# Kernel optimization log

Hardware: AMD Instinct MI355X
Metric: run time of the kernel (lower is better)

The kernel has to match this reference:

```python
import jax, jax.numpy as jnp
import numpy as np

SCALE = 1000.0
NEG = -1000000000.0
B, S, T, E, H = 64, 512, 96, 256, 512  # batch, src_len, trg_len, embed_dim, hidden_dim
ENC_DIM = 2 * H


def setup_inputs() -> dict:
    key = jax.random.key(0)
    def rn(i, shape):
        return jax.random.normal(jax.random.fold_in(key, i), shape, jnp.float32) / np.sqrt(shape[-1])
    inp = {}
    inp["src"] = jax.random.uniform(jax.random.fold_in(key, 100), (B, S), jnp.float32, 50.0, 1500.0)
    src_len = jax.random.randint(jax.random.fold_in(key, 101), (B,), S // 2, S + 1)
    inp["src_mask"] = (jnp.arange(S)[None, :] < src_len[:, None]).astype(jnp.int32)
    trg = jax.random.uniform(jax.random.fold_in(key, 102), (B, T), jnp.float32, 50.0, 1500.0)
    inp["trg"] = trg.at[:, 0].set(0.0)  # position 0 is the start sentinel
    trg_len = jax.random.randint(jax.random.fold_in(key, 103), (B,), T // 2, T + 1)
    inp["trg_mask"] = (jnp.arange(T)[None, :] < trg_len[:, None]).astype(jnp.int32)
    shapes = {
        "enc_proj_W": (E, 1), "enc_proj_b": (E,),
        "enc_Wih_f": (4 * H, E), "enc_Whh_f": (4 * H, H), "enc_bih_f": (4 * H,), "enc_bhh_f": (4 * H,),
        "enc_Wih_b": (4 * H, E), "enc_Whh_b": (4 * H, H), "enc_bih_b": (4 * H,), "enc_bhh_b": (4 * H,),
        "fc_h_W": (H, 2 * H), "fc_h_b": (H,), "fc_c_W": (H, 2 * H), "fc_c_b": (H,),
        "dec_proj_W": (E, 1), "dec_proj_b": (E,),
        "attn_Wenc": (H, ENC_DIM), "attn_Wdec": (H, H), "attn_v": (1, H),
        "dec_Wih": (4 * H, E + ENC_DIM), "dec_Whh": (4 * H, H), "dec_bih": (4 * H,), "dec_bhh": (4 * H,),
        "val_W": (1, H + ENC_DIM + E), "val_b": (1,),
        "stop_W": (1, H + ENC_DIM + E), "stop_b": (1,),
    }
    for i, (name, shp) in enumerate(shapes.items()):
        inp[name] = rn(i, shp)
    return inp


def _lstm_scan(x_tbe, m_tb1, Wih, Whh, bih, bhh, reverse):
    # Mask-gated LSTM scan == pack_padded_sequence semantics (padding at end):
    # state is frozen and outputs zeroed at padded steps; reverse=True gives the
    # backward direction of the bidirectional encoder.
    b, h = x_tbe.shape[1], Whh.shape[1]
    init = (jnp.zeros((b, h), x_tbe.dtype), jnp.zeros((b, h), x_tbe.dtype))
    bias = bih + bhh
    def step(carry, xm):
        hprev, cprev = carry
        xt, m = xm
        gates = xt @ Wih.T + hprev @ Whh.T + bias  # [B,4H], torch gate order i,f,g,o
        i, f, g, o = jnp.split(gates, 4, axis=-1)
        c_new = jax.nn.sigmoid(f) * cprev + jax.nn.sigmoid(i) * jnp.tanh(g)
        h_new = jax.nn.sigmoid(o) * jnp.tanh(c_new)
        hn = jnp.where(m, h_new, hprev)
        cn = jnp.where(m, c_new, cprev)
        return (hn, cn), jnp.where(m, h_new, 0.0)
    (hT, cT), outs = jax.lax.scan(step, init, (x_tbe, m_tb1), reverse=reverse)
    return outs, hT, cT


def _forward(src, trg, enc_proj_W, enc_proj_b, enc_Wih_f, enc_Whh_f, enc_bih_f, enc_bhh_f, enc_Wih_b, enc_Whh_b, enc_bih_b, enc_bhh_b, fc_h_W, fc_h_b, fc_c_W, fc_c_b, dec_proj_W, dec_proj_b, attn_Wenc, attn_Wdec, attn_v, dec_Wih, dec_Whh, dec_bih, dec_bhh, val_W, val_b, stop_W, stop_b, src_mask, trg_mask):
    src_norm = src / SCALE
    # ---- encoder (bidirectional, n_layers=1, dropout inactive in eval) ----
    emb = src_norm[..., None] * enc_proj_W[:, 0] + enc_proj_b  # Linear(1,E) -> [B,S,E]
    emb_t = jnp.transpose(emb, (1, 0, 2))                      # [S,B,E] time-major
    m_t = (src_mask.T > 0)[..., None]                          # [S,B,1]
    out_f, hF, cF = _lstm_scan(emb_t, m_t, enc_Wih_f, enc_Whh_f, enc_bih_f, enc_bhh_f, False)
    out_b, hB, cB = _lstm_scan(emb_t, m_t, enc_Wih_b, enc_Whh_b, enc_bih_b, enc_bhh_b, True)
    enc_outputs = jnp.transpose(jnp.concatenate([out_f, out_b], -1), (1, 0, 2))  # [B,S,2H]
    hidden = jnp.tanh(jnp.concatenate([hF, hB], -1) @ fc_h_W.T + fc_h_b)  # [B,H]
    cell = jnp.tanh(jnp.concatenate([cF, cB], -1) @ fc_c_W.T + fc_c_b)    # [B,H]
    # ---- decoder loop (full teacher forcing, ratio=1.0) ----
    eh = enc_outputs @ attn_Wenc.T  # [B,S,H], loop-invariant (same math, hoisted)
    valid = src_mask > 0            # [B,S]
    dec_bias = dec_bih + dec_bhh
    def dec_step(carry, x_t):
        h, c = carry
        energy = jnp.tanh((h @ attn_Wdec.T)[:, None, :] + eh)  # [B,S,H]
        scores = jnp.where(valid, energy @ attn_v[0], NEG)     # [B,S]
        w = jax.nn.softmax(scores, axis=1)
        context = jnp.einsum('bs,bse->be', w, enc_outputs)     # [B,2H]
        e = x_t[:, None] * dec_proj_W[:, 0] + dec_proj_b       # [B,E]
        gates = jnp.concatenate([e, context], -1) @ dec_Wih.T + h @ dec_Whh.T + dec_bias
        i, f, g, o = jnp.split(gates, 4, axis=-1)
        c_new = jax.nn.sigmoid(f) * c + jax.nn.sigmoid(i) * jnp.tanh(g)
        h_new = jax.nn.sigmoid(o) * jnp.tanh(c_new)
        feat = jnp.concatenate([h_new, context, e], -1)        # [B, H+2H+E]
        pv = feat @ val_W[0] + val_b[0]
        sl = feat @ stop_W[0] + stop_b[0]
        return (h_new, c_new), (pv * SCALE, sl)
    dec_in = (trg[:, :-1] / SCALE).T  # [T-1,B]: inputs for steps t=1..trg_len-1
    _, (pred_values, stop_logits) = jax.lax.scan(dec_step, (hidden, cell), dec_in)
    return pred_values.T, stop_logits.T  # each [B, T-1]


def reference(src, src_mask, trg, trg_mask, enc_proj_W, enc_proj_b, enc_Wih_f, enc_Whh_f, enc_bih_f, enc_bhh_f, enc_Wih_b, enc_Whh_b, enc_bih_b, enc_bhh_b, fc_h_W, fc_h_b, fc_c_W, fc_c_b, dec_proj_W, dec_proj_b, attn_Wenc, attn_Wdec, attn_v, dec_Wih, dec_Whh, dec_bih, dec_bhh, val_W, val_b, stop_W, stop_b):
    return _forward(src, trg, enc_proj_W, enc_proj_b, enc_Wih_f, enc_Whh_f, enc_bih_f, enc_bhh_f, enc_Wih_b, enc_Whh_b, enc_bih_b, enc_bhh_b, fc_h_W, fc_h_b, fc_c_W, fc_c_b, dec_proj_W, dec_proj_b, attn_Wenc, attn_Wdec, attn_v, dec_Wih, dec_Whh, dec_bih, dec_bhh, val_W, val_b, stop_W, stop_b, src_mask, trg_mask)
```

## Files before the change

kernel.cpp:

```cpp
#include <hip/hip_runtime.h>
#include <hip/hip_bf16.h>

#define AGENT __HIP_MEMORY_SCOPE_AGENT

typedef float f32x4 __attribute__((ext_vector_type(4)));
typedef short short8 __attribute__((ext_vector_type(8)));
union V16 { f32x4 f; short8 s; };


__device__ __forceinline__ float sigm(float x){ return 1.f/(1.f+__expf(-x)); }
__device__ __forceinline__ float tanhfast(float x){
  float ax = fabsf(x);
  float e = __expf(-2.f*ax);
  float r = (1.f-e)/(1.f+e);
  return copysignf(r, x);
}
__device__ __forceinline__ float dot4(float4 a, float4 b){
  return fmaf(a.x,b.x, fmaf(a.y,b.y, fmaf(a.z,b.z, a.w*b.w)));
}
__device__ __forceinline__ unsigned short bfbits(float x){
  return __bfloat16_as_ushort(__float2bfloat16(x));
}
__device__ __forceinline__ float bfu2f(unsigned short u){
  union{unsigned v; float f;} x; x.v = ((unsigned)u)<<16; return x.f;
}

__global__ void __launch_bounds__(256) precompute(
  const float* __restrict__ Wenc,
  const float* __restrict__ Wihf, const float* __restrict__ epW, const float* __restrict__ epb,
  const float* __restrict__ bihf, const float* __restrict__ bhhf,
  const float* __restrict__ Wihb, const float* __restrict__ bihb, const float* __restrict__ bhhb,
  const float* __restrict__ dWih, const float* __restrict__ dpW, const float* __restrict__ dpb,
  const float* __restrict__ dbih, const float* __restrict__ dbhh,
  const float* __restrict__ valW, const float* __restrict__ valb,
  const float* __restrict__ stopW, const float* __restrict__ stopb,
  float* __restrict__ PQ, float* __restrict__ WT, float* __restrict__ hc)
{
  const int idx = blockIdx.x*256 + threadIdx.x;
  if (idx < 524288){
    const int j = idx >> 9, n = idx & 511;
    WT[idx] = Wenc[(size_t)n*1024 + j];
  } else if (idx < 524288 + 6*2048){
    const int q = idx - 524288;
    const int set = q >> 11, j = q & 2047;
    const float* row; const float* vec; float add = 0.f;
    switch(set){
      case 0: row = Wihf + (size_t)j*256; vec = epW; break;
      case 1: row = Wihf + (size_t)j*256; vec = epb; add = bihf[j]+bhhf[j]; break;
      case 2: row = Wihb + (size_t)j*256; vec = epW; break;
      case 3: row = Wihb + (size_t)j*256; vec = epb; add = bihb[j]+bhhb[j]; break;
      case 4: row = dWih + (size_t)j*1280; vec = dpW; break;
      default: row = dWih + (size_t)j*1280; vec = dpb; add = dbih[j]+dbhh[j]; break;
    }
    float a = add;
    for (int e=0;e<256;e++) a = fmaf(row[e], vec[e], a);
    PQ[set*2048 + j] = a;
  } else if (idx < 524288 + 6*2048 + 4){
    const int q = idx - (524288 + 6*2048);
    const float* wrow = (q<2) ? valW : stopW;
    const float* vec  = (q&1) ? dpb : dpW;
    float a = (q&1) ? ((q<2)? valb[0] : stopb[0]) : 0.f;
    for (int e=0;e<256;e++) a = fmaf(wrow[1536+e], vec[e], a);
    hc[q] = a;
  }
}

__global__ void __launch_bounds__(512) wconv(
  const float* __restrict__ Whhf, const float* __restrict__ Whhb,
  const float* __restrict__ dWih, const float* __restrict__ dWhh,
  const float* __restrict__ Wdec, const float* __restrict__ Wenc,
  unsigned short* __restrict__ Wbf, unsigned short* __restrict__ Wcat,
  unsigned short* __restrict__ Wdecb, unsigned short* __restrict__ Wencb)
{
  const int i = blockIdx.x*512 + threadIdx.x;
  if (i < 2097152){
    const float v = (i < 1048576) ? Whhf[i] : Whhb[i-1048576];
    Wbf[i] = bfbits(v);
  } else if (i < 2097152+3145728){
    const int q = i - 2097152;
    const int r = q/1536, k = q - r*1536;
    const float v = (k<1024) ? dWih[(size_t)r*1280 + 256 + k] : dWhh[(size_t)r*512 + (k-1024)];
    Wcat[q] = bfbits(v);
  } else if (i < 2097152+3145728+262144){
    const int q = i - (2097152+3145728);
    Wdecb[q] = bfbits(Wdec[q]);
  } else if (i < 2097152+3145728+262144+524288){
    const int q = i - (2097152+3145728+262144);
    Wencb[q] = bfbits(Wenc[q]);
  }
}

__global__ void __launch_bounds__(512) enc_mfma(
    const float* __restrict__ src, const int* __restrict__ smask,
    const unsigned short* __restrict__ Wbf,
    const float* __restrict__ PQ,
    unsigned short* __restrict__ hbuf,
    float* __restrict__ hfin,
    float* __restrict__ cf, float* __restrict__ cb,
    __hip_bfloat16* __restrict__ enc,
    unsigned* __restrict__ cnt)
{
  __shared__ float hlds[16*256];
  __shared__ float red[4*64*4];
  __shared__ float gbuf[4*256];
  __shared__ alignas(16) unsigned short hstage[256];
  __shared__ alignas(16) unsigned short estage[256];

  const int tid = threadIdx.x;
  const int bid = blockIdx.x;
  const int dir = bid>>7, bhalf = (bid>>5)&3, us = bid&31;
  const int b0 = bhalf*16;
  unsigned* gcnt = cnt + (dir*4 + bhalf)*32;
  const int wv = tid>>6, lane = tid&63;
  const int nt = wv&3, kh = wv>>2;
  const int rowb = lane&15;

  short8 bfr[8];
  {
    const int g = nt*512 + us*16 + (lane&15);
    const unsigned short* wp = Wbf + ((size_t)dir*2048 + g)*512 + kh*256 + (lane>>4)*8;
    #pragma unroll
    for (int kt=0;kt<8;kt++) bfr[kt] = *(const short8*)(wp + kt*32);
  }

  float p0=0,p1=0,p2=0,p3=0,q0=0,q1=0,q2=0,q3=0;
  float creg = 0.f, hprev = 0.f;
  int bg = 0, ug = 0;
  if (tid < 256){
    bg = b0 + (tid>>4);
    ug = us*16 + (tid&15);
    const float* P = PQ + dir*4096; const float* Q = P + 2048;
    p0=P[ug]; p1=P[ug+512]; p2=P[ug+1024]; p3=P[ug+1536];
    q0=Q[ug]; q1=Q[ug+512]; q2=Q[ug+1024]; q3=Q[ug+1536];
  }

  for (int tt=0; tt<512; ++tt){
    const int t = dir ? (511-tt) : tt;
    if (tt>0){
      if (tid==0){
        while (__hip_atomic_load(gcnt, __ATOMIC_RELAXED, AGENT) < 32u*(unsigned)tt)
          __builtin_amdgcn_s_sleep(1);
      }
      __syncthreads();
      const int par = (tt-1)&1;
      f32x4 tmp0, tmp1;
      {
        const int f0 = tid, f1 = 512 + tid;
        const unsigned short* g0 = hbuf + (((size_t)(dir*2+par)*64 + b0 + (f0>>6))<<9) + (f0&63)*8;
        const unsigned short* g1 = hbuf + (((size_t)(dir*2+par)*64 + b0 + (f1>>6))<<9) + (f1&63)*8;
        asm volatile("global_load_dwordx4 %0, %1, off sc0 sc1" : "=v"(tmp0) : "v"(g0) : "memory");
        asm volatile("global_load_dwordx4 %0, %1, off sc0 sc1" : "=v"(tmp1) : "v"(g1) : "memory");
      }
      asm volatile("s_waitcnt vmcnt(0)" ::: "memory");
      __builtin_amdgcn_sched_barrier(0);
      {
        const int r0 = tid>>6, c0 = tid&63;
        *(f32x4*)&hlds[r0*256 + ((c0 ^ (r0&7))<<2)] = tmp0;
        const int r1 = (512+tid)>>6, c1 = tid&63;
        *(f32x4*)&hlds[r1*256 + ((c1 ^ (r1&7))<<2)] = tmp1;
      }
      __syncthreads();
    }

    f32x4 acc = {0.f,0.f,0.f,0.f};
    if (tt>0){
      #pragma unroll
      for (int kt=0; kt<8; ++kt){
        const int ch = (kh*8 + kt)*4 + (lane>>4);
        V16 a; a.f = *(const f32x4*)&hlds[rowb*256 + ((ch ^ (rowb&7))<<2)];
        acc = __builtin_amdgcn_mfma_f32_16x16x32_bf16(a.s, bfr[kt], acc, 0, 0, 0);
      }
    }
    if (kh==1) *(f32x4*)&red[(nt*64+lane)*4] = acc;
    __syncthreads();
    if (kh==0){
      const f32x4 o = *(const f32x4*)&red[(nt*64+lane)*4];
      #pragma unroll
      for (int i=0;i<4;i++){
        const int r = (lane>>4)*4 + i, c = lane&15;
        gbuf[nt*256 + r*16 + c] = acc[i] + o[i];
      }
    }
    __syncthreads();

    if (tid < 256){
      const float sx = src[bg*512+t]*0.001f;
      const int m = smask[bg*512+t];
      const float gi = gbuf[0*256+tid] + sx*p0 + q0;
      const float gf = gbuf[1*256+tid] + sx*p1 + q1;
      const float gg = gbuf[2*256+tid] + sx*p2 + q2;
      const float go = gbuf[3*256+tid] + sx*p3 + q3;
      const float cn = fmaf(sigm(gf), creg, sigm(gi)*tanhfast(gg));
      const float hn = sigm(go)*tanhfast(cn);
      const float hk = m ? hn : hprev;
      creg = m ? cn : creg;
      hprev = hk;
      hstage[tid] = bfbits(hk);
      estage[tid] = bfbits(m ? hn : 0.f);
    }
    __syncthreads();
    if (tid < 32){
      const int row = tid>>1, hw = tid&1;
      const f32x4 v = *(const f32x4*)(hstage + row*16 + hw*8);
      unsigned short* dst = hbuf + (((size_t)(dir*2+(tt&1))*64 + b0 + row)<<9) + us*16 + hw*8;
      asm volatile("global_store_dwordx4 %0, %1, off sc0 sc1" :: "v"(dst), "v"(v) : "memory");
    } else if (tid < 64){
      const int j = tid-32, row = j>>1, hw = j&1;
      const f32x4 v = *(const f32x4*)(estage + row*16 + hw*8);
      *(f32x4*)((unsigned short*)enc + ((size_t)((b0+row)*512 + t))*1024 + dir*512 + us*16 + hw*8) = v;
    }
    asm volatile("s_waitcnt vmcnt(0)" ::: "memory");
    __syncthreads();
    if (tid==0) __hip_atomic_fetch_add(gcnt, 1u, __ATOMIC_RELAXED, AGENT);
  }

  if (tid < 256){
    hfin[dir*32768 + bg*512 + ug] = hprev;
    (dir ? cb : cf)[bg*512 + ug] = creg;
  }
}

__global__ void __launch_bounds__(256) fc_init(
  const float* __restrict__ hf0, const float* __restrict__ hb0,
  const float* __restrict__ cf, const float* __restrict__ cb,
  const float* __restrict__ fchW, const float* __restrict__ fchB,
  const float* __restrict__ fccW, const float* __restrict__ fccB,
  float* __restrict__ dech, float* __restrict__ decc)
{
  const int which = blockIdx.x >> 7;
  const int wid = blockIdx.x & 127;
  const int b = threadIdx.x >> 2, ul = threadIdx.x & 3;
  const int u = wid*4 + ul;
  const float* s0 = which ? cf : hf0;
  const float* s1 = which ? cb : hb0;
  const float* W = which ? fccW : fchW;
  float acc = (which ? fccB : fchB)[u];
  const float4* x0 = (const float4*)(s0 + b*512);
  const float4* x1 = (const float4*)(s1 + b*512);
  const float4* wr = (const float4*)(W + (size_t)u*1024);
  #pragma unroll 4
  for (int k=0;k<128;k++) acc += dot4(x0[k], wr[k]);
  #pragma unroll 4
  for (int k=0;k<128;k++) acc += dot4(x1[k], wr[128+k]);
  (which ? decc : dech)[b*512+u] = tanhfast(acc);
}

__global__ void __launch_bounds__(256) eh_mfma(
  const unsigned short* __restrict__ enc,
  const unsigned short* __restrict__ Wencb,
  unsigned short* __restrict__ eh2)
{
  const int b = blockIdx.x>>6, st = (blockIdx.x>>3)&7, nt0 = blockIdx.x&7;
  const int wv = threadIdx.x>>6, lane = threadIdx.x&63;
  const int sA = st*64 + wv*16 + (lane&15);
  const int kb = (lane>>4)*8;
  const unsigned short* ap  = enc + ((size_t)(b*512 + sA))*1024 + kb;
  const unsigned short* bp0 = Wencb + ((size_t)(nt0*64 + (lane&15)))*1024 + kb;
  f32x4 acc[4] = {{0,0,0,0},{0,0,0,0},{0,0,0,0},{0,0,0,0}};
  for (int k0=0; k0<1024; k0+=32){
    V16 a; a.f = *(const f32x4*)(ap + k0);
    #pragma unroll
    for (int nt=0; nt<4; ++nt){
      V16 bb; bb.f = *(const f32x4*)(bp0 + (size_t)nt*16*1024 + k0);
      acc[nt] = __builtin_amdgcn_mfma_f32_16x16x32_bf16(a.s, bb.s, acc[nt], 0, 0, 0);
    }
  }
  const int sO = st*64 + wv*16 + (lane>>4)*4;
  const int col = lane&15;
  #pragma unroll
  for (int nt=0; nt<4; ++nt){
    #pragma unroll
    for (int i=0;i<4;i++){
      eh2[((size_t)(b*512 + sO + i))*512 + nt0*64 + nt*16 + col] = bfbits(acc[nt][i]);
    }
  }
}

__global__ void __launch_bounds__(256) enc_tr(
  const unsigned short* __restrict__ enc, unsigned short* __restrict__ encT2)
{
  __shared__ unsigned short tl[64][80];
  const int b = blockIdx.x>>7, st = (blockIdx.x>>4)&7, jt = blockIdx.x&15;
  const int r = threadIdx.x>>2, q = threadIdx.x&3;
  const unsigned short* src = enc + ((size_t)(b*512 + st*64 + r))*1024 + jt*64 + q*16;
  *(short8*)&tl[r][q*16]   = *(const short8*)src;
  *(short8*)&tl[r][q*16+8] = *(const short8*)(src+8);
  __syncthreads();
  unsigned short tmp[16];
  #pragma unroll
  for (int e=0;e<16;e++) tmp[e] = tl[q*16+e][r];
  unsigned short* dst = encT2 + ((size_t)(b*1024 + jt*64 + r))*512 + st*64 + q*16;
  *(short8*)dst     = *(short8*)&tmp[0];
  *(short8*)(dst+8) = *(short8*)&tmp[8];
}

template<int NG>
__device__ __forceinline__ void gbar(unsigned* gctr, unsigned* root, int grp, unsigned gen){
  asm volatile("s_waitcnt vmcnt(0)" ::: "memory");
  __syncthreads();
  if (threadIdx.x==0){
    const unsigned old = __hip_atomic_fetch_add(gctr + grp*32, 1u, __ATOMIC_RELAXED, AGENT);
    if (old == gen*16u - 1u)
      __hip_atomic_fetch_add(root, 1u, __ATOMIC_RELAXED, AGENT);
    while (__hip_atomic_load(root, __ATOMIC_RELAXED, AGENT) < gen*(unsigned)NG)
      __builtin_amdgcn_s_sleep(1);
  }
  __syncthreads();
}
template<int NB>
__device__ __forceinline__ void mbar(unsigned* mc, unsigned mgen){
  asm volatile("s_waitcnt vmcnt(0)" ::: "memory");
  __syncthreads();
  if (threadIdx.x==0){
    __hip_atomic_fetch_add(mc, 1u, __ATOMIC_RELAXED, AGENT);
    while (__hip_atomic_load(mc, __ATOMIC_RELAXED, AGENT) < mgen*(unsigned)NB)
      __builtin_amdgcn_s_sleep(1);
  }
  __syncthreads();
}

__global__ void __launch_bounds__(512) dec_fused256(
  const float* __restrict__ trg, const int* __restrict__ smask,
  const float* __restrict__ attnv,
  const unsigned short* __restrict__ eh2,
  const unsigned short* __restrict__ encT2,
  const unsigned short* __restrict__ Wcat,
  const unsigned short* __restrict__ Wdecb,
  const float* __restrict__ PQd, const float* __restrict__ hc,
  const float* __restrict__ valW, const float* __restrict__ stopW,
  const float* __restrict__ dech0, const float* __restrict__ decc0,
  float* __restrict__ scorep, float* __restrict__ ctxf,
  unsigned short* __restrict__ xbuf, float* __restrict__ gates,
  float* __restrict__ hcur, float* __restrict__ out,
  unsigned* __restrict__ gctr, unsigned* __restrict__ root, unsigned* __restrict__ mctr)
{
  __shared__ alignas(16) float redl[8192];
  __shared__ float vlds[512];
  __shared__ float hldsa[512];
  __shared__ float adhl[128];
  __shared__ float wlds[512];
  const int tid = threadIdx.x;
  const int bid = blockIdx.x;
  const int b = bid>>2, quad = bid&3;
  const int grp = bid>>4;
  const int lane = tid&63, wv = tid>>6;
  unsigned* mc = mctr + b*32;
  unsigned g = 0, m = 0;

  vlds[tid] = attnv[tid];

  short8 gw[6];
  if (bid < 128){
    const int n = bid*16 + (lane&15);
    const unsigned short* wp = Wcat + (size_t)n*1536 + wv*192 + (lane>>4)*8;
    #pragma unroll
    for (int ks=0;ks<6;ks++) gw[ks] = *(const short8*)(wp + ks*32);
  }

  const bool isb = (quad==0);
  float hr=0.f, cr=0.f;
  float pqi=0,pqf=0,pqg=0,pqo=0, qqi=0,qqf=0,qqg=0,qqo=0;
  float vwh=0,vwc0=0,vwc1=0, swh=0,swc0=0,swc1=0;
  if (isb){
    hr = dech0[b*512+tid]; cr = decc0[b*512+tid];
    pqi = PQd[tid];      pqf = PQd[512+tid];      pqg = PQd[1024+tid];      pqo = PQd[1536+tid];
    qqi = PQd[2048+tid]; qqf = PQd[2048+512+tid]; qqg = PQd[2048+1024+tid]; qqo = PQd[2048+1536+tid];
    vwh = valW[tid]; vwc0 = valW[512+tid]; vwc1 = valW[1024+tid];
    swh = stopW[tid]; swc0 = stopW[512+tid]; swc1 = stopW[1024+tid];
  }

  if (isb){
    const unsigned hb16 = (unsigned)bfbits(hr);
    unsigned short* xp = xbuf + b*1536 + 1024 + tid;
    asm volatile("global_store_short %0, %1, off sc0 sc1" :: "v"(xp), "v"(hb16) : "memory");
    float* hp = hcur + b*512 + tid;
    asm volatile("global_store_dword %0, %1, off sc0 sc1" :: "v"(hp), "v"(hr) : "memory");
  }
  ++m; mbar<4>(mc, m);

  for (int t=0; t<95; ++t){
    {
      float hv; const float* hp = hcur + b*512 + tid;
      asm volatile("global_load_dword %0, %1, off sc0 sc1\ns_waitcnt vmcnt(0)" : "=v"(hv) : "v"(hp) : "memory");
      hldsa[tid] = hv;
      __syncthreads();
      {
        const int jl = tid>>2, uc = tid&3;
        const unsigned short* wp = Wdecb + (size_t)(quad*128 + jl)*512 + uc*128;
        float a = 0.f;
        #pragma unroll
        for (int i=0;i<16;i++){
          const short8 w8 = *(const short8*)(wp + i*8);
          #pragma unroll
          for (int e=0;e<8;e++)
            a = fmaf(hldsa[uc*128 + i*8 + e], bfu2f((unsigned short)w8[e]), a);
        }
        redl[tid] = a;
      }
      __syncthreads();
      if (tid < 128)
        adhl[tid] = redl[tid*4] + redl[tid*4+1] + redl[tid*4+2] + redl[tid*4+3];
      __syncthreads();
      {
        const unsigned short* ep = eh2 + ((size_t)(b*512 + tid))*512 + quad*128;
        float part = 0.f;
        #pragma unroll
        for (int i=0;i<16;i++){
          const short8 e8 = *(const short8*)(ep + i*8);
          #pragma unroll
          for (int e=0;e<8;e++){
            const int n = i*8 + e;
            part = fmaf(vlds[quad*128+n], tanhfast(adhl[n] + bfu2f((unsigned short)e8[e])), part);
          }
        }
        float* sp = scorep + (size_t)bid*512 + tid;
        asm volatile("global_store_dword %0, %1, off sc0 sc1" :: "v"(sp), "v"(part) : "memory");
      }
    }
    ++m; mbar<4>(mc, m);

    {
      float pa, pb, pc, pd;
      const float* pp = scorep + (size_t)(b*4)*512 + tid;
      asm volatile("global_load_dword %0, %1, off sc0 sc1" : "=v"(pa) : "v"(pp) : "memory");
      asm volatile("global_load_dword %0, %1, off sc0 sc1" : "=v"(pb) : "v"(pp+512) : "memory");
      asm volatile("global_load_dword %0, %1, off sc0 sc1" : "=v"(pc) : "v"(pp+1024) : "memory");
      asm volatile("global_load_dword %0, %1, off sc0 sc1" : "=v"(pd) : "v"(pp+1536) : "memory");
      asm volatile("s_waitcnt vmcnt(0)" ::: "memory");
      __builtin_amdgcn_sched_barrier(0);
      float s0 = (pa+pb)+(pc+pd);
      s0 = smask[b*512+tid] ? s0 : -1.0e9f;
      redl[512+tid] = s0;
      __syncthreads();
      for (int off=256; off>0; off>>=1){
        if (tid<off) redl[512+tid] = fmaxf(redl[512+tid], redl[512+tid+off]);
        __syncthreads();
      }
      const float mx = redl[512];
      __syncthreads();
      const float e = __expf(s0 - mx);
      redl[512+tid] = e;
      __syncthreads();
      for (int off=256; off>0; off>>=1){
        if (tid<off) redl[512+tid] += redl[512+tid+off];
        __syncthreads();
      }
      const float Z = redl[512];
      __syncthreads();
      wlds[tid] = e / Z;
      __syncthreads();
      {
        const int jj = tid>>1, sh = tid&1;
        const unsigned short* cp = encT2 + ((size_t)(b*1024 + quad*256 + jj))*512 + sh*256;
        float c = 0.f;
        #pragma unroll
        for (int i=0;i<32;i++){
          const short8 c8 = *(const short8*)(cp + i*8);
          #pragma unroll
          for (int e2=0;e2<8;e2++)
            c = fmaf(wlds[sh*256 + i*8 + e2], bfu2f((unsigned short)c8[e2]), c);
        }
        redl[tid] = c;
      }
      __syncthreads();
      if (tid < 256){
        const float cv = redl[tid*2] + redl[tid*2+1];
        const int j = quad*256 + tid;
        float* cp2 = ctxf + b*1024 + j;
        asm volatile("global_store_dword %0, %1, off sc0 sc1" :: "v"(cp2), "v"(cv) : "memory");
        const unsigned cb16 = (unsigned)bfbits(cv);
        unsigned short* xp = xbuf + b*1536 + j;
        asm volatile("global_store_short %0, %1, off sc0 sc1" :: "v"(xp), "v"(cb16) : "memory");
      }
    }
    ++g; gbar<16>(gctr, root, grp, g);

    if (bid < 128){
      f32x4 av[2][6];
      f32x4 acc[4] = {{0,0,0,0},{0,0,0,0},{0,0,0,0},{0,0,0,0}};
      {
        const unsigned short* xp0 = xbuf + (size_t)(lane&15)*1536 + wv*192 + (lane>>4)*8;
        #pragma unroll
        for (int ks=0;ks<6;ks++){
          const unsigned short* p = xp0 + ks*32;
          asm volatile("global_load_dwordx4 %0, %1, off sc0 sc1" : "=v"(av[0][ks]) : "v"(p) : "memory");
        }
      }
      #pragma unroll
      for (int mt=0; mt<4; ++mt){
        if (mt<3){
          const unsigned short* xpn = xbuf + (size_t)((mt+1)*16 + (lane&15))*1536 + wv*192 + (lane>>4)*8;
          #pragma unroll
          for (int ks=0;ks<6;ks++){
            const unsigned short* p = xpn + ks*32;
            asm volatile("global_load_dwordx4 %0, %1, off sc0 sc1" : "=v"(av[(mt+1)&1][ks]) : "v"(p) : "memory");
          }
          asm volatile("s_waitcnt vmcnt(6)" ::: "memory");
        } else {
          asm volatile("s_waitcnt vmcnt(0)" ::: "memory");
        }
        __builtin_amdgcn_sched_barrier(0);
        #pragma unroll
        for (int ks=0;ks<6;ks++){
          V16 a; a.f = av[mt&1][ks];
          acc[mt] = __builtin_amdgcn_mfma_f32_16x16x32_bf16(a.s, gw[ks], acc[mt], 0, 0, 0);
        }
      }
      #pragma unroll
      for (int mt=0; mt<4; ++mt)
        *(f32x4*)&redl[wv*1024 + lane*16 + mt*4] = acc[mt];
    }
    __syncthreads();
    if (bid < 128){
      #pragma unroll
      for (int h2=0; h2<2; ++h2){
        const int o = h2*512 + tid;
        const int ob = o>>4, col = o&15;
        const int mt = ob>>4, row = ob&15;
        const int base = (((row>>2)<<4) | col)*16 + mt*4 + (row&3);
        float gsum = 0.f;
        #pragma unroll
        for (int w2=0; w2<8; ++w2) gsum += redl[w2*1024 + base];
        float* gp = gates + ob*2048 + bid*16 + col;
        asm volatile("global_store_dword %0, %1, off sc0 sc1" :: "v"(gp), "v"(gsum) : "memory");
      }
    }
    ++g; gbar<16>(gctr, root, grp, g);

    if (isb){
      float g4[4], c0v, c1v;
      {
        const float* gp = gates + b*2048 + tid;
        const float* cp = ctxf + b*1024 + tid;
        asm volatile("global_load_dword %0, %1, off sc0 sc1" : "=v"(g4[0]) : "v"(gp) : "memory");
        asm volatile("global_load_dword %0, %1, off sc0 sc1" : "=v"(g4[1]) : "v"(gp+512) : "memory");
        asm volatile("global_load_dword %0, %1, off sc0 sc1" : "=v"(g4[2]) : "v"(gp+1024) : "memory");
        asm volatile("global_load_dword %0, %1, off sc0 sc1" : "=v"(g4[3]) : "v"(gp+1536) : "memory");
        asm volatile("global_load_dword %0, %1, off sc0 sc1" : "=v"(c0v) : "v"(cp) : "memory");
        asm volatile("global_load_dword %0, %1, off sc0 sc1" : "=v"(c1v) : "v"(cp+512) : "memory");
        asm volatile("s_waitcnt vmcnt(0)" ::: "memory");
        __builtin_amdgcn_sched_barrier(0);
      }
      const float x = trg[b*96 + t]*0.001f;
      const float gi = g4[0] + x*pqi + qqi;
      const float gf = g4[1] + x*pqf + qqf;
      const float gg = g4[2] + x*pqg + qqg;
      const float go = g4[3] + x*pqo + qqo;
      const float cn = fmaf(sigm(gf), cr, sigm(gi)*tanhfast(gg));
      const float hn = sigm(go)*tanhfast(cn);
      cr = cn; hr = hn;
      const unsigned hb16 = (unsigned)bfbits(hn);
      unsigned short* xp = xbuf + b*1536 + 1024 + tid;
      asm volatile("global_store_short %0, %1, off sc0 sc1" :: "v"(xp), "v"(hb16) : "memory");
      float* hp = hcur + b*512 + tid;
      asm volatile("global_store_dword %0, %1, off sc0 sc1" :: "v"(hp), "v"(hn) : "memory");
      redl[512+tid]  = fmaf(hn, vwh, fmaf(c0v, vwc0, c1v*vwc1));
      redl[1024+tid] = fmaf(hn, swh, fmaf(c0v, swc0, c1v*swc1));
      __syncthreads();
      for (int off=256; off>0; off>>=1){
        if (tid<off){ redl[512+tid]+=redl[512+tid+off]; redl[1024+tid]+=redl[1024+tid+off]; }
        __syncthreads();
      }
      if (tid==0){
        out[b*95 + t] = (redl[512] + x*hc[0] + hc[1])*1000.f;
        out[6080 + b*95 + t] = redl[1024] + x*hc[2] + hc[3];
      }
    }
    ++m; mbar<4>(mc, m);
  }
}

__global__ void __launch_bounds__(512, 4) dec_fused512(
  const float* __restrict__ trg, const int* __restrict__ smask,
  const float* __restrict__ attnv,
  const unsigned short* __restrict__ eh2,
  const unsigned short* __restrict__ encT2,
  const unsigned short* __restrict__ Wcat,
  const unsigned short* __restrict__ Wdecb,
  const float* __restrict__ PQd, const float* __restrict__ hc,
  const float* __restrict__ valW, const float* __restrict__ stopW,
  const float* __restrict__ dech0, const float* __restrict__ decc0,
  float* __restrict__ scorep, float* __restrict__ ctxf,
  unsigned short* __restrict__ xbuf, float* __restrict__ gates,
  float* __restrict__ hcur, float* __restrict__ out,
  unsigned* __restrict__ gctr, unsigned* __restrict__ root, unsigned* __restrict__ mctr)
{
  __shared__ unsigned short eh2l[32768];
  __shared__ alignas(16) float redl[2048];
  __shared__ float vlds[512];
  __shared__ float adhl[64];
  __shared__ int slen_sh;
  const int tid = threadIdx.x;
  const int bid = blockIdx.x;
  const int b = bid>>3, oct = bid&7;
  const int grp = bid>>4;
  const int lane = tid&63, wv = tid>>6;
  unsigned* mc = mctr + b*32;
  unsigned g = 0, m = 0;

  vlds[tid] = attnv[tid];

  redl[tid] = (float)smask[b*512+tid];
  __syncthreads();
  for (int off=256; off>0; off>>=1){
    if (tid<off) redl[tid] += redl[tid+off];
    __syncthreads();
  }
  if (tid==0) slen_sh = (int)(redl[0]+0.5f);
  __syncthreads();
  const int slen = slen_sh;
  const int nch = (slen + 127) >> 7;

  {
    const unsigned short* ep = eh2 + ((size_t)(b*512 + tid))*512 + oct*64;
    short8 r8[8];
    #pragma unroll
    for (int i=0;i<8;i++) r8[i] = *(const short8*)(ep + i*8);
    #pragma unroll
    for (int i=0;i<8;i++)
      #pragma unroll
      for (int e=0;e<8;e++)
        eh2l[(i*8+e)*512 + tid] = (unsigned short)r8[i][e];
  }
  __syncthreads();

  short8 gw[6];
  if (bid < 128){
    const int n = bid*16 + (lane&15);
    const unsigned short* wp = Wcat + (size_t)n*1536 + wv*192 + (lane>>4)*8;
    #pragma unroll
    for (int ks=0;ks<6;ks++) gw[ks] = *(const short8*)(wp + ks*32);
  }

  const bool isb = (oct==0);
  float hr=0.f, cr=0.f;
  float pqi=0,pqf=0,pqg=0,pqo=0, qqi=0,qqf=0,qqg=0,qqo=0;
  float vwh=0,vwc0=0,vwc1=0, swh=0,swc0=0,swc1=0;
  if (isb){
    hr = dech0[b*512+tid]; cr = decc0[b*512+tid];
    pqi = PQd[tid];      pqf = PQd[512+tid];      pqg = PQd[1024+tid];      pqo = PQd[1536+tid];
    qqi = PQd[2048+tid]; qqf = PQd[2048+512+tid]; qqg = PQd[2048+1024+tid]; qqo = PQd[2048+1536+tid];
    vwh = valW[tid]; vwc0 = valW[512+tid]; vwc1 = valW[1024+tid];
    swh = stopW[tid]; swc0 = stopW[512+tid]; swc1 = stopW[1024+tid];
  }

  if (isb){
    const unsigned hb16 = (unsigned)bfbits(hr);
    unsigned short* xp = xbuf + b*1536 + 1024 + tid;
    asm volatile("global_store_short %0, %1, off sc0 sc1" :: "v"(xp), "v"(hb16) : "memory");
    float* hp = hcur + b*512 + tid;
    asm volatile("global_store_dword %0, %1, off sc0 sc1" :: "v"(hp), "v"(hr) : "memory");
  }
  ++m; mbar<8>(mc, m);

  for (int t=0; t<95; ++t){
    {
      float hv; const float* hp = hcur + b*512 + tid;
      asm volatile("global_load_dword %0, %1, off sc0 sc1\ns_waitcnt vmcnt(0)" : "=v"(hv) : "v"(hp) : "memory");
      redl[1024+tid] = hv;
      __syncthreads();
      {
        const int jl = tid>>3, uc = tid&7;
        const unsigned short* wp = Wdecb + (size_t)(oct*64 + jl)*512 + uc*64;
        float a = 0.f;
        #pragma unroll
        for (int i=0;i<8;i++){
          const short8 w8 = *(const short8*)(wp + i*8);
          #pragma unroll
          for (int e=0;e<8;e++)
            a = fmaf(redl[1024 + uc*64 + i*8 + e], bfu2f((unsigned short)w8[e]), a);
        }
        redl[tid] = a;
      }
      __syncthreads();
      if (tid < 64){
        float s8 = 0.f;
        #pragma unroll
        for (int i=0;i<8;i++) s8 += redl[tid*8+i];
        adhl[tid] = s8;
      }
      __syncthreads();
      {
        float part = 0.f;
        #pragma unroll 8
        for (int n=0;n<64;++n)
          part = fmaf(vlds[oct*64+n], tanhfast(adhl[n] + bfu2f(eh2l[n*512 + tid])), part);
        float* sp = scorep + (size_t)bid*512 + tid;
        asm volatile("global_store_dword %0, %1, off sc0 sc1" :: "v"(sp), "v"(part) : "memory");
      }
    }
    ++m; mbar<8>(mc, m);

    {
      float ps[8];
      const float* pp = scorep + (size_t)(b*8)*512 + tid;
      #pragma unroll
      for (int i=0;i<8;i++){
        const float* p = pp + i*512;
        asm volatile("global_load_dword %0, %1, off sc0 sc1" : "=v"(ps[i]) : "v"(p) : "memory");
      }
      const int jj = tid>>2, sh = tid&3;
      const bool act = (sh < nch);
      const int she = act ? sh : 0;
      const unsigned short* cp = encT2 + ((size_t)(b*1024 + oct*128 + jj))*512 + she*128;
      f32x4 pre[8];
      #pragma unroll
      for (int i=0;i<8;i++){
        const unsigned short* p = cp + i*8;
        asm volatile("global_load_dwordx4 %0, %1, off" : "=v"(pre[i]) : "v"(p) : "memory");
      }
      asm volatile("s_waitcnt vmcnt(8)" ::: "memory");
      __builtin_amdgcn_sched_barrier(0);
      float s0 = ((ps[0]+ps[1])+(ps[2]+ps[3]))+((ps[4]+ps[5])+(ps[6]+ps[7]));
      s0 = (tid < slen) ? s0 : -1.0e9f;
      redl[512+tid] = s0;
      __syncthreads();
      for (int off=256; off>0; off>>=1){
        if (tid<off) redl[512+tid] = fmaxf(redl[512+tid], redl[512+tid+off]);
        __syncthreads();
      }
      const float mx = redl[512];
      __syncthreads();
      const float e = __expf(s0 - mx);
      redl[512+tid] = e;
      __syncthreads();
      for (int off=256; off>0; off>>=1){
        if (tid<off) redl[512+tid] += redl[512+tid+off];
        __syncthreads();
      }
      const float Z = redl[512];
      __syncthreads();
      redl[1024+tid] = e / Z;
      __syncthreads();
      float c = 0.f;
      asm volatile("s_waitcnt vmcnt(0)" ::: "memory");
      __builtin_amdgcn_sched_barrier(0);
      #pragma unroll
      for (int i=0;i<8;i++){
        V16 x; x.f = pre[i];
        #pragma unroll
        for (int e2=0;e2<8;e2++)
          c = fmaf(redl[1024 + she*128 + i*8 + e2], bfu2f((unsigned short)x.s[e2]), c);
      }
      #pragma unroll
      for (int i=8;i<16;i++){
        const short8 c8 = *(const short8*)(cp + i*8);
        #pragma unroll
        for (int e2=0;e2<8;e2++)
          c = fmaf(redl[1024 + she*128 + i*8 + e2], bfu2f((unsigned short)c8[e2]), c);
      }
      c = act ? c : 0.f;
      redl[tid] = c;
      __syncthreads();
      if (tid < 128){
        const float cv = redl[tid*4] + redl[tid*4+1] + redl[tid*4+2] + redl[tid*4+3];
        const int j = oct*128 + tid;
        float* cp2 = ctxf + b*1024 + j;
        asm volatile("global_store_dword %0, %1, off sc0 sc1" :: "v"(cp2), "v"(cv) : "memory");
        const unsigned cb16 = (unsigned)bfbits(cv);
        unsigned short* xp = xbuf + b*1536 + j;
        asm volatile("global_store_short %0, %1, off sc0 sc1" :: "v"(xp), "v"(cb16) : "memory");
      }
    }
    ++g; gbar<32>(gctr, root, grp, g);

    redl[tid] = 0.f; redl[512+tid] = 0.f;
    __syncthreads();
    if (bid < 128){
      f32x4 av[2][6];
      f32x4 acc[4] = {{0,0,0,0},{0,0,0,0},{0,0,0,0},{0,0,0,0}};
      {
        const unsigned short* xp0 = xbuf + (size_t)(lane&15)*1536 + wv*192 + (lane>>4)*8;
        #pragma unroll
        for (int ks=0;ks<6;ks++){
          const unsigned short* p = xp0 + ks*32;
          asm volatile("global_load_dwordx4 %0, %1, off sc0 sc1" : "=v"(av[0][ks]) : "v"(p) : "memory");
        }
      }
      #pragma unroll
      for (int mt=0; mt<4; ++mt){
        if (mt<3){
          const unsigned short* xpn = xbuf + (size_t)((mt+1)*16 + (lane&15))*1536 + wv*192 + (lane>>4)*8;
          #pragma unroll
          for (int ks=0;ks<6;ks++){
            const unsigned short* p = xpn + ks*32;
            asm volatile("global_load_dwordx4 %0, %1, off sc0 sc1" : "=v"(av[(mt+1)&1][ks]) : "v"(p) : "memory");
          }
          asm volatile("s_waitcnt vmcnt(6)" ::: "memory");
        } else {
          asm volatile("s_waitcnt vmcnt(0)" ::: "memory");
        }
        __builtin_amdgcn_sched_barrier(0);
        #pragma unroll
        for (int ks=0;ks<6;ks++){
          V16 a; a.f = av[mt&1][ks];
          acc[mt] = __builtin_amdgcn_mfma_f32_16x16x32_bf16(a.s, gw[ks], acc[mt], 0, 0, 0);
        }
      }
      #pragma unroll
      for (int mt=0; mt<4; ++mt)
        #pragma unroll
        for (int i=0;i<4;i++){
          const int r = (lane>>4)*4 + i, cc = lane&15;
          atomicAdd(&redl[(mt*16 + r)*16 + cc], acc[mt][i]);
        }
    }
    __syncthreads();
    if (bid < 128){
      #pragma unroll
      for (int h2=0; h2<2; ++h2){
        const int o = h2*512 + tid;
        const int ob = o>>4, col = o&15;
        const float gsum = redl[o];
        float* gp = gates + ob*2048 + bid*16 + col;
        asm volatile("global_store_dword %0, %1, off sc0 sc1" :: "v"(gp), "v"(gsum) : "memory");
      }
    }
    ++g; gbar<32>(gctr, root, grp, g);

    if (isb){
      float g4[4], c0v, c1v;
      {
        const float* gp = gates + b*2048 + tid;
        const float* cp = ctxf + b*1024 + tid;
        asm volatile("global_load_dword %0, %1, off sc0 sc1" : "=v"(g4[0]) : "v"(gp) : "memory");
        asm volatile("global_load_dword %0, %1, off sc0 sc1" : "=v"(g4[1]) : "v"(gp+512) : "memory");
        asm volatile("global_load_dword %0, %1, off sc0 sc1" : "=v"(g4[2]) : "v"(gp+1024) : "memory");
        asm volatile("global_load_dword %0, %1, off sc0 sc1" : "=v"(g4[3]) : "v"(gp+1536) : "memory");
        asm volatile("global_load_dword %0, %1, off sc0 sc1" : "=v"(c0v) : "v"(cp) : "memory");
        asm volatile("global_load_dword %0, %1, off sc0 sc1" : "=v"(c1v) : "v"(cp+512) : "memory");
        asm volatile("s_waitcnt vmcnt(0)" ::: "memory");
        __builtin_amdgcn_sched_barrier(0);
      }
      const float x = trg[b*96 + t]*0.001f;
      const float gi = g4[0] + x*pqi + qqi;
      const float gf = g4[1] + x*pqf + qqf;
      const float gg = g4[2] + x*pqg + qqg;
      const float go = g4[3] + x*pqo + qqo;
      const float cn = fmaf(sigm(gf), cr, sigm(gi)*tanhfast(gg));
      const float hn = sigm(go)*tanhfast(cn);
      cr = cn; hr = hn;
      const unsigned hb16 = (unsigned)bfbits(hn);
      unsigned short* xp = xbuf + b*1536 + 1024 + tid;
      asm volatile("global_store_short %0, %1, off sc0 sc1" :: "v"(xp), "v"(hb16) : "memory");
      float* hp = hcur + b*512 + tid;
      asm volatile("global_store_dword %0, %1, off sc0 sc1" :: "v"(hp), "v"(hn) : "memory");
      redl[512+tid]  = fmaf(hn, vwh, fmaf(c0v, vwc0, c1v*vwc1));
      redl[1024+tid] = fmaf(hn, swh, fmaf(c0v, swc0, c1v*swc1));
      __syncthreads();
      for (int off=256; off>0; off>>=1){
        if (tid<off){ redl[512+tid]+=redl[512+tid+off]; redl[1024+tid]+=redl[1024+tid+off]; }
        __syncthreads();
      }
      if (tid==0){
        out[b*95 + t] = (redl[512] + x*hc[0] + hc[1])*1000.f;
        out[6080 + b*95 + t] = redl[1024] + x*hc[2] + hc[3];
      }
    }
    ++m; mbar<8>(mc, m);
  }
}

extern "C" void kernel_launch(void* const* d_in, const int* in_sizes, int n_in,
                              void* d_out, int out_size, void* d_ws, size_t ws_size,
                              hipStream_t stream)
{
  (void)in_sizes; (void)n_in; (void)out_size; (void)ws_size;
  const float* src   = (const float*)d_in[0];
  const int*   smask = (const int*)  d_in[1];
  const float* trg   = (const float*)d_in[2];
  const float* epW   = (const float*)d_in[4];
  const float* epb   = (const float*)d_in[5];
  const float* Wihf  = (const float*)d_in[6];
  const float* Whhf  = (const float*)d_in[7];
  const float* bihf  = (const float*)d_in[8];
  const float* bhhf  = (const float*)d_in[9];
  const float* Wihb  = (const float*)d_in[10];
  const float* Whhb  = (const float*)d_in[11];
  const float* bihb  = (const float*)d_in[12];
  const float* bhhb  = (const float*)d_in[13];
  const float* fchW  = (const float*)d_in[14];
  const float* fchB  = (const float*)d_in[15];
  const float* fccW  = (const float*)d_in[16];
  const float* fccB  = (const float*)d_in[17];
  const float* dpW   = (const float*)d_in[18];
  const float* dpb   = (const float*)d_in[19];
  const float* Wenc  = (const float*)d_in[20];
  const float* Wdec  = (const float*)d_in[21];
  const float* attnv = (const float*)d_in[22];
  const float* dWih  = (const float*)d_in[23];
  const float* dWhh  = (const float*)d_in[24];
  const float* dbih  = (const float*)d_in[25];
  const float* dbhh  = (const float*)d_in[26];
  const float* valW  = (const float*)d_in[27];
  const float* valb  = (const float*)d_in[28];
  const float* stopW = (const float*)d_in[29];
  const float* stopb = (const float*)d_in[30];
  float* out = (float*)d_out;

  char* ws = (char*)d_ws;
  size_t off = 0;
  auto take = [&](size_t nbytes) -> char* {
    char* p = ws + off;
    off += (nbytes + 255) & ~(size_t)255;
    return p;
  };
  unsigned short* enc   = (unsigned short*)take((size_t)64*512*1024*2);
  unsigned short* eh2   = (unsigned short*)take((size_t)64*512*512*2);
  unsigned short* encT2 = (unsigned short*)take((size_t)64*1024*512*2);
  unsigned short* hbuf  = (unsigned short*)take(2*2*64*512*2);
  unsigned short* Wbf   = (unsigned short*)take((size_t)2*2048*512*2);
  unsigned short* Wcat  = (unsigned short*)take((size_t)2048*1536*2);
  unsigned short* Wdecb = (unsigned short*)take(512*512*2);
  unsigned short* Wencb = (unsigned short*)take(512*1024*2);
  float* WT    = (float*)take((size_t)1024*512*4);
  float* hfin  = (float*)take(2*64*512*4);
  float* cf    = (float*)take(64*512*4);
  float* cb    = (float*)take(64*512*4);
  float* PQ    = (float*)take(6*2048*4);
  float* dech0 = (float*)take(64*512*4);
  float* decc0 = (float*)take(64*512*4);
  float* scorep= (float*)take(512*512*4);
  float* ctxf  = (float*)take(64*1024*4);
  unsigned short* xbuf = (unsigned short*)take(64*1536*2);
  float* gates = (float*)take(64*2048*4);
  float* hcur  = (float*)take(64*512*4);
  float* hc    = (float*)take(256);
  unsigned* cnt  = (unsigned*)take(1024);
  unsigned* gctr = (unsigned*)take(4096);
  unsigned* root = (unsigned*)take(256);
  unsigned* mctr = (unsigned*)take(8192);
  float* PQd = PQ + 8192;
  (void)hipMemsetAsync(cnt, 0, 1024+4096+256+8192, stream);

  precompute<<<2097, 256, 0, stream>>>(Wenc, Wihf, epW, epb, bihf, bhhf, Wihb, bihb, bhhb,
                                       dWih, dpW, dpb, dbih, dbhh, valW, valb, stopW, stopb,
                                       PQ, WT, hc);
  wconv<<<11776, 512, 0, stream>>>(Whhf, Whhb, dWih, dWhh, Wdec, Wenc, Wbf, Wcat, Wdecb, Wencb);

  {
    void* args[] = { (void*)&src, (void*)&smask, (void*)&Wbf, (void*)&PQ,
                     (void*)&hbuf, (void*)&hfin, (void*)&cf, (void*)&cb, (void*)&enc, (void*)&cnt };
    (void)hipLaunchCooperativeKernel((void*)enc_mfma, dim3(256), dim3(512), args, 0, stream);
  }

  {
    const float* hfF = hfin;
    const float* hbF = hfin + 32768;
    fc_init<<<256, 256, 0, stream>>>(hfF, hbF, cf, cb, fchW, fchB, fccW, fccB, dech0, decc0);
  }
  eh_mfma<<<4096, 256, 0, stream>>>(enc, Wencb, eh2);
  enc_tr<<<8192, 256, 0, stream>>>(enc, encT2);

  {
    void* args[] = { (void*)&trg, (void*)&smask, (void*)&attnv,
                     (void*)&eh2, (void*)&encT2, (void*)&Wcat, (void*)&Wdecb,
                     (void*)&PQd, (void*)&hc, (void*)&valW, (void*)&stopW,
                     (void*)&dech0, (void*)&decc0,
                     (void*)&scorep, (void*)&ctxf,
                     (void*)&xbuf, (void*)&gates, (void*)&hcur, (void*)&out,
                     (void*)&gctr, (void*)&root, (void*)&mctr };
    int nb2 = 0;
    (void)hipOccupancyMaxActiveBlocksPerMultiprocessor(&nb2, dec_fused512, 512, 0);
    hipError_t e512 = hipErrorUnknown;
    if (nb2 >= 2)
      e512 = hipLaunchCooperativeKernel((void*)dec_fused512, dim3(512), dim3(512), args, 0, stream);
    if (e512 != hipSuccess)
      (void)hipLaunchCooperativeKernel((void*)dec_fused256, dim3(256), dim3(512), args, 0, stream);
  }
}
```

Measured before the change: 7.093 ms.

## Replace atomic-counter barriers with per-block flag barriers and redundant LSTM cell update

In the 512-block decoder, the hierarchical atomic-counter grid barrier and the per-batch counter barrier are replaced with flag-array barriers. Each block stores its generation to its own padded slot, and each thread polls one peer's slot. All eight blocks of a batch now compute the LSTM cell update redundantly and keep the hidden state in LDS. This removes the extra end-of-step batch barrier and the global hcur store/reload. The cost is more polling traffic (512 loads per grid barrier per block) and duplicated gate loads and transcendentals across blocks.

```diff
diff --git a/kernel.cpp b/kernel.cpp
--- a/kernel.cpp
+++ b/kernel.cpp
@@ -319,6 +319,35 @@
   __syncthreads();
 }
 
+__device__ __forceinline__ void fgbar(unsigned* aflag, unsigned gen){
+  asm volatile("s_waitcnt vmcnt(0)" ::: "memory");
+  __syncthreads();
+  if (threadIdx.x==0)
+    __hip_atomic_store(aflag + (size_t)blockIdx.x*32, gen, __ATOMIC_RELAXED, AGENT);
+  {
+    unsigned v = __hip_atomic_load(aflag + (size_t)threadIdx.x*32, __ATOMIC_RELAXED, AGENT);
+    while (v < gen){
+      __builtin_amdgcn_s_sleep(2);
+      v = __hip_atomic_load(aflag + (size_t)threadIdx.x*32, __ATOMIC_RELAXED, AGENT);
+    }
+  }
+  __syncthreads();
+}
+__device__ __forceinline__ void fmbar(unsigned* mflag, int b, int oct, unsigned gen){
+  asm volatile("s_waitcnt vmcnt(0)" ::: "memory");
+  __syncthreads();
+  if (threadIdx.x==0)
+    __hip_atomic_store(mflag + (size_t)(b*8+oct)*32, gen, __ATOMIC_RELAXED, AGENT);
+  if (threadIdx.x < 8){
+    unsigned v = __hip_atomic_load(mflag + (size_t)(b*8+(int)threadIdx.x)*32, __ATOMIC_RELAXED, AGENT);
+    while (v < gen){
+      __builtin_amdgcn_s_sleep(1);
+      v = __hip_atomic_load(mflag + (size_t)(b*8+(int)threadIdx.x)*32, __ATOMIC_RELAXED, AGENT);
+    }
+  }
+  __syncthreads();
+}
+
 __global__ void __launch_bounds__(512) dec_fused256(
   const float* __restrict__ trg, const int* __restrict__ smask,
   const float* __restrict__ attnv,
@@ -332,7 +361,8 @@
   float* __restrict__ scorep, float* __restrict__ ctxf,
   unsigned short* __restrict__ xbuf, float* __restrict__ gates,
   float* __restrict__ hcur, float* __restrict__ out,
-  unsigned* __restrict__ gctr, unsigned* __restrict__ root, unsigned* __restrict__ mctr)
+  unsigned* __restrict__ gctr, unsigned* __restrict__ root, unsigned* __restrict__ mctr,
+  unsigned* __restrict__ aflag, unsigned* __restrict__ mflag)
 {
   __shared__ alignas(16) float redl[8192];
   __shared__ float vlds[512];
@@ -346,6 +376,7 @@
   const int lane = tid&63, wv = tid>>6;
   unsigned* mc = mctr + b*32;
   unsigned g = 0, m = 0;
+  (void)aflag; (void)mflag;
 
   vlds[tid] = attnv[tid];
 
@@ -583,20 +614,21 @@
   float* __restrict__ scorep, float* __restrict__ ctxf,
   unsigned short* __restrict__ xbuf, float* __restrict__ gates,
   float* __restrict__ hcur, float* __restrict__ out,
-  unsigned* __restrict__ gctr, unsigned* __restrict__ root, unsigned* __restrict__ mctr)
+  unsigned* __restrict__ gctr, unsigned* __restrict__ root, unsigned* __restrict__ mctr,
+  unsigned* __restrict__ aflag, unsigned* __restrict__ mflag)
 {
   __shared__ unsigned short eh2l[32768];
   __shared__ alignas(16) float redl[2048];
   __shared__ float vlds[512];
+  __shared__ float hl[512];
   __shared__ float adhl[64];
   __shared__ int slen_sh;
   const int tid = threadIdx.x;
   const int bid = blockIdx.x;
   const int b = bid>>3, oct = bid&7;
-  const int grp = bid>>4;
   const int lane = tid&63, wv = tid>>6;
-  unsigned* mc = mctr + b*32;
   unsigned g = 0, m = 0;
+  (void)gctr; (void)root; (void)mctr; (void)hcur;
 
   vlds[tid] = attnv[tid];
 
@@ -622,7 +654,6 @@
       for (int e=0;e<8;e++)
         eh2l[(i*8+e)*512 + tid] = (unsigned short)r8[i][e];
   }
-  __syncthreads();
 
   short8 gw[6];
   if (bid < 128){
@@ -633,32 +664,28 @@
   }
 
   const bool isb = (oct==0);
-  float hr=0.f, cr=0.f;
-  float pqi=0,pqf=0,pqg=0,pqo=0, qqi=0,qqf=0,qqg=0,qqo=0;
+  float cr = decc0[b*512+tid];
+  const float pqi = PQd[tid],      pqf = PQd[512+tid],      pqg = PQd[1024+tid],      pqo = PQd[1536+tid];
+  const float qqi = PQd[2048+tid], qqf = PQd[2048+512+tid], qqg = PQd[2048+1024+tid], qqo = PQd[2048+1536+tid];
   float vwh=0,vwc0=0,vwc1=0, swh=0,swc0=0,swc1=0;
   if (isb){
-    hr = dech0[b*512+tid]; cr = decc0[b*512+tid];
-    pqi = PQd[tid];      pqf = PQd[512+tid];      pqg = PQd[1024+tid];      pqo = PQd[1536+tid];
-    qqi = PQd[2048+tid]; qqf = PQd[2048+512+tid]; qqg = PQd[2048+1024+tid]; qqo = PQd[2048+1536+tid];
     vwh = valW[tid]; vwc0 = valW[512+tid]; vwc1 = valW[1024+tid];
     swh = stopW[tid]; swc0 = stopW[512+tid]; swc1 = stopW[1024+tid];
   }
 
-  if (isb){
-    const unsigned hb16 = (unsigned)bfbits(hr);
-    unsigned short* xp = xbuf + b*1536 + 1024 + tid;
-    asm volatile("global_store_short %0, %1, off sc0 sc1" :: "v"(xp), "v"(hb16) : "memory");
-    float* hp = hcur + b*512 + tid;
-    asm volatile("global_store_dword %0, %1, off sc0 sc1" :: "v"(hp), "v"(hr) : "memory");
-  }
-  ++m; mbar<8>(mc, m);
+  {
+    const float h0 = dech0[b*512+tid];
+    hl[tid] = h0;
+    if (isb){
+      const unsigned hb16 = (unsigned)bfbits(h0);
+      unsigned short* xp = xbuf + b*1536 + 1024 + tid;
+      asm volatile("global_store_short %0, %1, off sc0 sc1" :: "v"(xp), "v"(hb16) : "memory");
+    }
+  }
+  __syncthreads();
 
   for (int t=0; t<95; ++t){
     {
-      float hv; const float* hp = hcur + b*512 + tid;
-      asm volatile("global_load_dword %0, %1, off sc0 sc1\ns_waitcnt vmcnt(0)" : "=v"(hv) : "v"(hp) : "memory");
-      redl[1024+tid] = hv;
-      __syncthreads();
       {
         const int jl = tid>>3, uc = tid&7;
         const unsigned short* wp = Wdecb + (size_t)(oct*64 + jl)*512 + uc*64;
@@ -668,7 +695,7 @@
           const short8 w8 = *(const short8*)(wp + i*8);
           #pragma unroll
           for (int e=0;e<8;e++)
-            a = fmaf(redl[1024 + uc*64 + i*8 + e], bfu2f((unsigned short)w8[e]), a);
+            a = fmaf(hl[uc*64 + i*8 + e], bfu2f((unsigned short)w8[e]), a);
         }
         redl[tid] = a;
       }
@@ -689,7 +716,7 @@
         asm volatile("global_store_dword %0, %1, off sc0 sc1" :: "v"(sp), "v"(part) : "memory");
       }
     }
-    ++m; mbar<8>(mc, m);
+    ++m; fmbar(mflag, b, oct, m);
 
     {
       float ps[8];
@@ -762,7 +789,7 @@
         asm volatile("global_store_short %0, %1, off sc0 sc1" :: "v"(xp), "v"(cb16) : "memory");
       }
     }
-    ++g; gbar<32>(gctr, root, grp, g);
+    ++g; fgbar(aflag, g);
 
     redl[tid] = 0.f; redl[512+tid] = 0.f;
     __syncthreads();
@@ -816,19 +843,21 @@
         asm volatile("global_store_dword %0, %1, off sc0 sc1" :: "v"(gp), "v"(gsum) : "memory");
       }
     }
-    ++g; gbar<32>(gctr, root, grp, g);
-
-    if (isb){
-      float g4[4], c0v, c1v;
+    ++g; fgbar(aflag, g);
+
+    {
+      float g4[4], c0v = 0.f, c1v = 0.f;
       {
         const float* gp = gates + b*2048 + tid;
-        const float* cp = ctxf + b*1024 + tid;
         asm volatile("global_load_dword %0, %1, off sc0 sc1" : "=v"(g4[0]) : "v"(gp) : "memory");
         asm volatile("global_load_dword %0, %1, off sc0 sc1" : "=v"(g4[1]) : "v"(gp+512) : "memory");
         asm volatile("global_load_dword %0, %1, off sc0 sc1" : "=v"(g4[2]) : "v"(gp+1024) : "memory");
         asm volatile("global_load_dword %0, %1, off sc0 sc1" : "=v"(g4[3]) : "v"(gp+1536) : "memory");
-        asm volatile("global_load_dword %0, %1, off sc0 sc1" : "=v"(c0v) : "v"(cp) : "memory");
-        asm volatile("global_load_dword %0, %1, off sc0 sc1" : "=v"(c1v) : "v"(cp+512) : "memory");
+        if (isb){
+          const float* cp = ctxf + b*1024 + tid;
+          asm volatile("global_load_dword %0, %1, off sc0 sc1" : "=v"(c0v) : "v"(cp) : "memory");
+          asm volatile("global_load_dword %0, %1, off sc0 sc1" : "=v"(c1v) : "v"(cp+512) : "memory");
+        }
         asm volatile("s_waitcnt vmcnt(0)" ::: "memory");
         __builtin_amdgcn_sched_barrier(0);
       }
@@ -839,25 +868,27 @@
       const float go = g4[3] + x*pqo + qqo;
       const float cn = fmaf(sigm(gf), cr, sigm(gi)*tanhfast(gg));
       const float hn = sigm(go)*tanhfast(cn);
-      cr = cn; hr = hn;
-      const unsigned hb16 = (unsigned)bfbits(hn);
-      unsigned short* xp = xbuf + b*1536 + 1024 + tid;
-      asm volatile("global_store_short %0, %1, off sc0 sc1" :: "v"(xp), "v"(hb16) : "memory");
-      float* hp = hcur + b*512 + tid;
-      asm volatile("global_store_dword %0, %1, off sc0 sc1" :: "v"(hp), "v"(hn) : "memory");
-      redl[512+tid]  = fmaf(hn, vwh, fmaf(c0v, vwc0, c1v*vwc1));
-      redl[1024+tid] = fmaf(hn, swh, fmaf(c0v, swc0, c1v*swc1));
-      __syncthreads();
-      for (int off=256; off>0; off>>=1){
-        if (tid<off){ redl[512+tid]+=redl[512+tid+off]; redl[1024+tid]+=redl[1024+tid+off]; }
+      cr = cn;
+      __syncthreads();
+      hl[tid] = hn;
+      if (isb){
+        const unsigned hb16 = (unsigned)bfbits(hn);
+        unsigned short* xp = xbuf + b*1536 + 1024 + tid;
+        asm volatile("global_store_short %0, %1, off sc0 sc1" :: "v"(xp), "v"(hb16) : "memory");
+        redl[512+tid]  = fmaf(hn, vwh, fmaf(c0v, vwc0, c1v*vwc1));
+        redl[1024+tid] = fmaf(hn, swh, fmaf(c0v, swc0, c1v*swc1));
         __syncthreads();
-      }
-      if (tid==0){
-        out[b*95 + t] = (redl[512] + x*hc[0] + hc[1])*1000.f;
-        out[6080 + b*95 + t] = redl[1024] + x*hc[2] + hc[3];
-      }
-    }
-    ++m; mbar<8>(mc, m);
+        for (int off=256; off>0; off>>=1){
+          if (tid<off){ redl[512+tid]+=redl[512+tid+off]; redl[1024+tid]+=redl[1024+tid+off]; }
+          __syncthreads();
+        }
+        if (tid==0){
+          out[b*95 + t] = (redl[512] + x*hc[0] + hc[1])*1000.f;
+          out[6080 + b*95 + t] = redl[1024] + x*hc[2] + hc[3];
+        }
+      }
+      __syncthreads();
+    }
   }
 }
 
@@ -930,8 +961,10 @@
   unsigned* gctr = (unsigned*)take(4096);
   unsigned* root = (unsigned*)take(256);
   unsigned* mctr = (unsigned*)take(8192);
+  unsigned* aflag = (unsigned*)take(65536);
+  unsigned* mflag = (unsigned*)take(65536);
   float* PQd = PQ + 8192;
-  (void)hipMemsetAsync(cnt, 0, 1024+4096+256+8192, stream);
+  (void)hipMemsetAsync(cnt, 0, 1024+4096+256+8192+65536+65536, stream);
 
   precompute<<<2097, 256, 0, stream>>>(Wenc, Wihf, epW, epb, bihf, bhhf, Wihb, bihb, bhhb,
                                        dWih, dpW, dpb, dbih, dbhh, valW, valb, stopW, stopb,
@@ -959,7 +992,8 @@
                      (void*)&dech0, (void*)&decc0,
                      (void*)&scorep, (void*)&ctxf,
                      (void*)&xbuf, (void*)&gates, (void*)&hcur, (void*)&out,
-                     (void*)&gctr, (void*)&root, (void*)&mctr };
+                     (void*)&gctr, (void*)&root, (void*)&mctr,
+                     (void*)&aflag, (void*)&mflag };
     int nb2 = 0;
     (void)hipOccupancyMaxActiveBlocksPerMultiprocessor(&nb2, dec_fused512, 512, 0);
     hipError_t e512 = hipErrorUnknown;
```

After: 7.010 ms. Within noise of the previous version (-1.2%).
